# Kernel tuning notes

Measured on AMD Instinct MI355X. Metric: run time of the kernel, lower is better.

The kernel has to match this reference:

```python
import jax, jax.numpy as jnp
import numpy as np


def _kabsch_rmsd(p, c):
    # p, c: [N, 3]
    pm = jnp.mean(p, axis=0)  # [3]
    cm = jnp.mean(c, axis=0)  # [3]
    # 3x3 cross-covariance
    A = (p - pm).T @ (c - cm)
    U, S, Vt = jnp.linalg.svd(A, full_matrices=False)
    d = jnp.sign(jnp.linalg.det(A))
    # corr_mat = diag([1, 1, d]);  rotation = U @ corr_mat @ Vt
    scale = jnp.concatenate([jnp.ones((2,), dtype=p.dtype), d[None].astype(p.dtype)])
    R = U @ (scale[:, None] * Vt)  # [3,3]
    # translation = pm - R @ cm; aligned coords = (R @ c^T)^T + translation
    aligned = c @ R.T + (pm - R @ cm)
    sq = jnp.sum((p - aligned) ** 2, axis=1)  # [N]
    return jnp.sqrt(jnp.mean(sq))


def setup_inputs() -> dict:
    key = jax.random.key(0)
    k1, k2 = jax.random.split(key)
    B, N = 4096, 2048
    coords_pred = jax.random.normal(k1, (B, N, 3), dtype=jnp.float32)
    coords = jax.random.normal(k2, (B, N, 3), dtype=jnp.float32)
    return {"coords_pred": coords_pred, "coords": coords}


def reference(coords_pred, coords):
    # Batched Kabsch alignment + RMSD; default mode='global', return_all=False
    # -> mean over the per-sample RMSDs.
    rmsds = jax.vmap(_kabsch_rmsd)(coords_pred, coords)  # [B]
    return jnp.mean(rmsds)
```

## Files before the change

### kernel.cpp

```cpp
#include <hip/hip_runtime.h>
#include <math.h>

#define NPTS 2048
#define BLOCK 256
#define BPB 4
#define CHUNKS (NPTS / (64 * 4))

__global__ __launch_bounds__(BLOCK, 4) void kabsch_kernel(
    const float* __restrict__ P, const float* __restrict__ C,
    float* __restrict__ out, int B) {
  const int wave = threadIdx.x >> 6;
  const int lane = threadIdx.x & 63;
  const int b = blockIdx.x * BPB + wave;

  double rmsd = 0.0;
  if (b < B) {
    const float4* p4 = (const float4*)(P + (size_t)b * (NPTS * 3));
    const float4* c4 = (const float4*)(C + (size_t)b * (NPTS * 3));

    float acc[17];
#pragma unroll
    for (int i = 0; i < 17; i++) acc[i] = 0.f;

#define ACCUM(PA, PB, PQ, CA, CB, CQ)                                   \
  do {                                                                  \
    const float Px[4] = {PA.x, PA.w, PB.z, PQ.y};                       \
    const float Py[4] = {PA.y, PB.x, PB.w, PQ.z};                       \
    const float Pz[4] = {PA.z, PB.y, PQ.x, PQ.w};                       \
    const float Cx[4] = {CA.x, CA.w, CB.z, CQ.y};                       \
    const float Cy[4] = {CA.y, CB.x, CB.w, CQ.z};                       \
    const float Cz[4] = {CA.z, CB.y, CQ.x, CQ.w};                       \
    _Pragma("unroll")                                                   \
    for (int i = 0; i < 4; i++) {                                       \
      const float px = Px[i], py = Py[i], pz = Pz[i];                   \
      const float cx = Cx[i], cy = Cy[i], cz = Cz[i];                   \
      acc[0] += px; acc[1] += py; acc[2] += pz;                         \
      acc[3] += cx; acc[4] += cy; acc[5] += cz;                         \
      acc[6] += px * px + py * py + pz * pz;                            \
      acc[7] += cx * cx + cy * cy + cz * cz;                            \
      acc[8]  += px * cx; acc[9]  += px * cy; acc[10] += px * cz;       \
      acc[11] += py * cx; acc[12] += py * cy; acc[13] += py * cz;       \
      acc[14] += pz * cx; acc[15] += pz * cy; acc[16] += pz * cz;       \
    }                                                                   \
  } while (0)

    int base = 3 * lane;
    float4 pa = p4[base], pb = p4[base + 1], pq = p4[base + 2];
    float4 ca = c4[base], cb = c4[base + 1], cq = c4[base + 2];
#pragma unroll
    for (int k = 0; k < CHUNKS - 1; k++) {
      base += 64 * 3;
      const float4 npa = p4[base], npb = p4[base + 1], npq = p4[base + 2];
      const float4 nca = c4[base], ncb = c4[base + 1], ncq = c4[base + 2];
      __builtin_amdgcn_sched_barrier(0);
      ACCUM(pa, pb, pq, ca, cb, cq);
      pa = npa; pb = npb; pq = npq;
      ca = nca; cb = ncb; cq = ncq;
    }
    ACCUM(pa, pb, pq, ca, cb, cq);

#pragma unroll
    for (int off = 32; off > 0; off >>= 1) {
#pragma unroll
      for (int i = 0; i < 17; i++) acc[i] += __shfl_down(acc[i], off);
    }

    if (lane == 0) {
      double s[17];
#pragma unroll
      for (int i = 0; i < 17; i++) s[i] = (double)acc[i];
      const double invN = 1.0 / (double)NPTS;
      const double spx = s[0], spy = s[1], spz = s[2];
      const double scx = s[3], scy = s[4], scz = s[5];
      const double Ep = s[6] - (spx * spx + spy * spy + spz * spz) * invN;
      const double Ec = s[7] - (scx * scx + scy * scy + scz * scz) * invN;
      const double a00 = s[8]  - spx * scx * invN, a01 = s[9]  - spx * scy * invN, a02 = s[10] - spx * scz * invN;
      const double a10 = s[11] - spy * scx * invN, a11 = s[12] - spy * scy * invN, a12 = s[13] - spy * scz * invN;
      const double a20 = s[14] - spz * scx * invN, a21 = s[15] - spz * scy * invN, a22 = s[16] - spz * scz * invN;
      const double det = a00 * (a11 * a22 - a12 * a21)
                       - a01 * (a10 * a22 - a12 * a20)
                       + a02 * (a10 * a21 - a11 * a20);
      const double b00 = a00 * a00 + a10 * a10 + a20 * a20;
      const double b11 = a01 * a01 + a11 * a11 + a21 * a21;
      const double b22 = a02 * a02 + a12 * a12 + a22 * a22;
      const double b01 = a00 * a01 + a10 * a11 + a20 * a21;
      const double b02 = a00 * a02 + a10 * a12 + a20 * a22;
      const double b12 = a01 * a02 + a11 * a12 + a21 * a22;
      const double q = (b00 + b11 + b22) / 3.0;
      const double p1 = b01 * b01 + b02 * b02 + b12 * b12;
      const double d0 = b00 - q, d1 = b11 - q, d2 = b22 - q;
      const double p2 = d0 * d0 + d1 * d1 + d2 * d2 + 2.0 * p1;
      double e1, e2, e3;
      if (p2 < 1e-30) {
        e1 = e2 = e3 = q;
      } else {
        const double pp = sqrt(p2 / 6.0);
        const double inv = 1.0 / pp;
        const double c00 = d0 * inv, c11 = d1 * inv, c22 = d2 * inv;
        const double c01 = b01 * inv, c02 = b02 * inv, c12 = b12 * inv;
        double r = 0.5 * (c00 * (c11 * c22 - c12 * c12)
                        - c01 * (c01 * c22 - c12 * c02)
                        + c02 * (c01 * c12 - c11 * c02));
        r = fmin(1.0, fmax(-1.0, r));
        const double phi = acos(r) / 3.0;
        e1 = q + 2.0 * pp * cos(phi);
        e3 = q + 2.0 * pp * cos(phi + 2.0943951023931953);
        e2 = 3.0 * q - e1 - e3;
      }
      const double s1 = sqrt(fmax(e1, 0.0));
      const double s2 = sqrt(fmax(e2, 0.0));
      const double s3 = sqrt(fmax(e3, 0.0));
      const double dsign = (det > 0.0) ? 1.0 : ((det < 0.0) ? -1.0 : 0.0);
      const double trRS = s1 + s2 + dsign * s3;
      const double msd = (Ep + Ec - 2.0 * trRS) * invN;
      rmsd = sqrt(fmax(msd, 0.0));
    }
  }

  __shared__ double red[BPB];
  if (lane == 0) red[wave] = rmsd;
  __syncthreads();
  if (threadIdx.x == 0) {
    const double sum = red[0] + red[1] + red[2] + red[3];
    atomicAdd(out, (float)(sum / (double)B));
  }
}

extern "C" void kernel_launch(void* const* d_in, const int* in_sizes, int n_in,
                              void* d_out, int out_size, void* d_ws, size_t ws_size,
                              hipStream_t stream) {
  const float* P = (const float*)d_in[0];
  const float* C = (const float*)d_in[1];
  float* out = (float*)d_out;
  const int B = in_sizes[0] / (NPTS * 3);
  hipMemsetAsync(out, 0, sizeof(float), stream);
  kabsch_kernel<<<(B + BPB - 1) / BPB, BLOCK, 0, stream>>>(P, C, out, B);
}
```

Before: 217.2 us.

## Stage inputs through LDS with async global_load_lds double buffering

Replaces direct per-lane float4 global loads with global_load_lds transfers into per-wave double-buffered LDS, then reads each lane's 12 contiguous floats from LDS. Each wave now processes two batch samples sequentially, halving the grid, and launch bounds drop to 2 blocks per CU because of the 48KB LDS footprint. The intent is to keep more bytes in flight and get coalesced wide loads. The costs are an extra LDS round trip, manual waitcnt management, and lower occupancy on a kernel that is memory-bound.

```diff
diff --git a/kernel.cpp b/kernel.cpp
--- a/kernel.cpp
+++ b/kernel.cpp
@@ -3,24 +3,27 @@
 
 #define NPTS 2048
 #define BLOCK 256
-#define BPB 4
-#define CHUNKS (NPTS / (64 * 4))
+#define NW 4
+#define NB 2
+#define CHUNK_F 768
+#define NCHUNK (NPTS * 3 / CHUNK_F)
 
-__global__ __launch_bounds__(BLOCK, 4) void kabsch_kernel(
+#define GLD_LDS(gp, lp)                                                       \
+  __builtin_amdgcn_global_load_lds(                                           \
+      (const __attribute__((address_space(1))) void*)(gp),                    \
+      (__attribute__((address_space(3))) void*)(lp), 16, 0, 0)
+
+__global__ __launch_bounds__(BLOCK, 2) void kabsch_kernel(
     const float* __restrict__ P, const float* __restrict__ C,
     float* __restrict__ out, int B) {
   const int wave = threadIdx.x >> 6;
   const int lane = threadIdx.x & 63;
-  const int b = blockIdx.x * BPB + wave;
 
-  double rmsd = 0.0;
-  if (b < B) {
-    const float4* p4 = (const float4*)(P + (size_t)b * (NPTS * 3));
-    const float4* c4 = (const float4*)(C + (size_t)b * (NPTS * 3));
+  __shared__ float lds[NW][2][2 * CHUNK_F];
+  float* const buf0 = &lds[wave][0][0];
+  float* const buf1 = &lds[wave][1][0];
 
-    float acc[17];
-#pragma unroll
-    for (int i = 0; i < 17; i++) acc[i] = 0.f;
+  double rmsd_sum = 0.0;
 
 #define ACCUM(PA, PB, PQ, CA, CB, CQ)                                   \
   do {                                                                  \
@@ -44,81 +47,111 @@
     }                                                                   \
   } while (0)
 
-    int base = 3 * lane;
-    float4 pa = p4[base], pb = p4[base + 1], pq = p4[base + 2];
-    float4 ca = c4[base], cb = c4[base + 1], cq = c4[base + 2];
+#define STAGE(dst, kk)                                                  \
+  do {                                                                  \
+    const float* ps = pB + (kk) * CHUNK_F + lane * 4;                   \
+    const float* cs = cB + (kk) * CHUNK_F + lane * 4;                   \
+    GLD_LDS(ps,       (dst));                                           \
+    GLD_LDS(ps + 256, (dst) + 256);                                     \
+    GLD_LDS(ps + 512, (dst) + 512);                                     \
+    GLD_LDS(cs,       (dst) + 768);                                     \
+    GLD_LDS(cs + 256, (dst) + 1024);                                    \
+    GLD_LDS(cs + 512, (dst) + 1280);                                    \
+  } while (0)
+
+  for (int it = 0; it < NB; ++it) {
+    const int b = (blockIdx.x * NW + wave) * NB + it;
+    if (b < B) {
+      const float* pB = P + (size_t)b * (NPTS * 3);
+      const float* cB = C + (size_t)b * (NPTS * 3);
+
+      float acc[17];
 #pragma unroll
-    for (int k = 0; k < CHUNKS - 1; k++) {
-      base += 64 * 3;
-      const float4 npa = p4[base], npb = p4[base + 1], npq = p4[base + 2];
-      const float4 nca = c4[base], ncb = c4[base + 1], ncq = c4[base + 2];
-      __builtin_amdgcn_sched_barrier(0);
-      ACCUM(pa, pb, pq, ca, cb, cq);
-      pa = npa; pb = npb; pq = npq;
-      ca = nca; cb = ncb; cq = ncq;
-    }
-    ACCUM(pa, pb, pq, ca, cb, cq);
+      for (int i = 0; i < 17; i++) acc[i] = 0.f;
+
+      STAGE(buf0, 0);
+#pragma unroll
+      for (int k = 0; k < NCHUNK; ++k) {
+        float* const cur = (k & 1) ? buf1 : buf0;
+        float* const nxt = (k & 1) ? buf0 : buf1;
+        if (k + 1 < NCHUNK) {
+          asm volatile("s_waitcnt lgkmcnt(0)" ::: "memory");
+          STAGE(nxt, k + 1);
+          asm volatile("s_waitcnt vmcnt(6)" ::: "memory");
+        } else {
+          asm volatile("s_waitcnt vmcnt(0)" ::: "memory");
+        }
+        __builtin_amdgcn_sched_barrier(0);
+        const float4 pa = *(const float4*)(cur + 12 * lane);
+        const float4 pb = *(const float4*)(cur + 12 * lane + 4);
+        const float4 pq = *(const float4*)(cur + 12 * lane + 8);
+        const float4 ca = *(const float4*)(cur + 768 + 12 * lane);
+        const float4 cb = *(const float4*)(cur + 768 + 12 * lane + 4);
+        const float4 cq = *(const float4*)(cur + 768 + 12 * lane + 8);
+        ACCUM(pa, pb, pq, ca, cb, cq);
+      }
 
 #pragma unroll
-    for (int off = 32; off > 0; off >>= 1) {
+      for (int off = 32; off > 0; off >>= 1) {
 #pragma unroll
-      for (int i = 0; i < 17; i++) acc[i] += __shfl_down(acc[i], off);
-    }
+        for (int i = 0; i < 17; i++) acc[i] += __shfl_down(acc[i], off);
+      }
 
-    if (lane == 0) {
-      double s[17];
+      if (lane == 0) {
+        double s[17];
 #pragma unroll
-      for (int i = 0; i < 17; i++) s[i] = (double)acc[i];
-      const double invN = 1.0 / (double)NPTS;
-      const double spx = s[0], spy = s[1], spz = s[2];
-      const double scx = s[3], scy = s[4], scz = s[5];
-      const double Ep = s[6] - (spx * spx + spy * spy + spz * spz) * invN;
-      const double Ec = s[7] - (scx * scx + scy * scy + scz * scz) * invN;
-      const double a00 = s[8]  - spx * scx * invN, a01 = s[9]  - spx * scy * invN, a02 = s[10] - spx * scz * invN;
-      const double a10 = s[11] - spy * scx * invN, a11 = s[12] - spy * scy * invN, a12 = s[13] - spy * scz * invN;
-      const double a20 = s[14] - spz * scx * invN, a21 = s[15] - spz * scy * invN, a22 = s[16] - spz * scz * invN;
-      const double det = a00 * (a11 * a22 - a12 * a21)
-                       - a01 * (a10 * a22 - a12 * a20)
-                       + a02 * (a10 * a21 - a11 * a20);
-      const double b00 = a00 * a00 + a10 * a10 + a20 * a20;
-      const double b11 = a01 * a01 + a11 * a11 + a21 * a21;
-      const double b22 = a02 * a02 + a12 * a12 + a22 * a22;
-      const double b01 = a00 * a01 + a10 * a11 + a20 * a21;
-      const double b02 = a00 * a02 + a10 * a12 + a20 * a22;
-      const double b12 = a01 * a02 + a11 * a12 + a21 * a22;
-      const double q = (b00 + b11 + b22) / 3.0;
-      const double p1 = b01 * b01 + b02 * b02 + b12 * b12;
-      const double d0 = b00 - q, d1 = b11 - q, d2 = b22 - q;
-      const double p2 = d0 * d0 + d1 * d1 + d2 * d2 + 2.0 * p1;
-      double e1, e2, e3;
-      if (p2 < 1e-30) {
-        e1 = e2 = e3 = q;
-      } else {
-        const double pp = sqrt(p2 / 6.0);
-        const double inv = 1.0 / pp;
-        const double c00 = d0 * inv, c11 = d1 * inv, c22 = d2 * inv;
-        const double c01 = b01 * inv, c02 = b02 * inv, c12 = b12 * inv;
-        double r = 0.5 * (c00 * (c11 * c22 - c12 * c12)
-                        - c01 * (c01 * c22 - c12 * c02)
-                        + c02 * (c01 * c12 - c11 * c02));
-        r = fmin(1.0, fmax(-1.0, r));
-        const double phi = acos(r) / 3.0;
-        e1 = q + 2.0 * pp * cos(phi);
-        e3 = q + 2.0 * pp * cos(phi + 2.0943951023931953);
-        e2 = 3.0 * q - e1 - e3;
+        for (int i = 0; i < 17; i++) s[i] = (double)acc[i];
+        const double invN = 1.0 / (double)NPTS;
+        const double spx = s[0], spy = s[1], spz = s[2];
+        const double scx = s[3], scy = s[4], scz = s[5];
+        const double Ep = s[6] - (spx * spx + spy * spy + spz * spz) * invN;
+        const double Ec = s[7] - (scx * scx + scy * scy + scz * scz) * invN;
+        const double a00 = s[8]  - spx * scx * invN, a01 = s[9]  - spx * scy * invN, a02 = s[10] - spx * scz * invN;
+        const double a10 = s[11] - spy * scx * invN, a11 = s[12] - spy * scy * invN, a12 = s[13] - spy * scz * invN;
+        const double a20 = s[14] - spz * scx * invN, a21 = s[15] - spz * scy * invN, a22 = s[16] - spz * scz * invN;
+        const double det = a00 * (a11 * a22 - a12 * a21)
+                         - a01 * (a10 * a22 - a12 * a20)
+                         + a02 * (a10 * a21 - a11 * a20);
+        const double b00 = a00 * a00 + a10 * a10 + a20 * a20;
+        const double b11 = a01 * a01 + a11 * a11 + a21 * a21;
+        const double b22 = a02 * a02 + a12 * a12 + a22 * a22;
+        const double b01 = a00 * a01 + a10 * a11 + a20 * a21;
+        const double b02 = a00 * a02 + a10 * a12 + a20 * a22;
+        const double b12 = a01 * a02 + a11 * a12 + a21 * a22;
+        const double q = (b00 + b11 + b22) / 3.0;
+        const double p1 = b01 * b01 + b02 * b02 + b12 * b12;
+        const double d0 = b00 - q, d1 = b11 - q, d2 = b22 - q;
+        const double p2 = d0 * d0 + d1 * d1 + d2 * d2 + 2.0 * p1;
+        double e1, e2, e3;
+        if (p2 < 1e-30) {
+          e1 = e2 = e3 = q;
+        } else {
+          const double pp = sqrt(p2 / 6.0);
+          const double inv = 1.0 / pp;
+          const double c00 = d0 * inv, c11 = d1 * inv, c22 = d2 * inv;
+          const double c01 = b01 * inv, c02 = b02 * inv, c12 = b12 * inv;
+          double r = 0.5 * (c00 * (c11 * c22 - c12 * c12)
+                          - c01 * (c01 * c22 - c12 * c02)
+                          + c02 * (c01 * c12 - c11 * c02));
+          r = fmin(1.0, fmax(-1.0, r));
+          const double phi = acos(r) / 3.0;
+          e1 = q + 2.0 * pp * cos(phi);
+          e3 = q + 2.0 * pp * cos(phi + 2.0943951023931953);
+          e2 = 3.0 * q - e1 - e3;
+        }
+        const double s1 = sqrt(fmax(e1, 0.0));
+        const double s2 = sqrt(fmax(e2, 0.0));
+        const double s3 = sqrt(fmax(e3, 0.0));
+        const double dsign = (det > 0.0) ? 1.0 : ((det < 0.0) ? -1.0 : 0.0);
+        const double trRS = s1 + s2 + dsign * s3;
+        const double msd = (Ep + Ec - 2.0 * trRS) * invN;
+        rmsd_sum += sqrt(fmax(msd, 0.0));
       }
-      const double s1 = sqrt(fmax(e1, 0.0));
-      const double s2 = sqrt(fmax(e2, 0.0));
-      const double s3 = sqrt(fmax(e3, 0.0));
-      const double dsign = (det > 0.0) ? 1.0 : ((det < 0.0) ? -1.0 : 0.0);
-      const double trRS = s1 + s2 + dsign * s3;
-      const double msd = (Ep + Ec - 2.0 * trRS) * invN;
-      rmsd = sqrt(fmax(msd, 0.0));
     }
   }
 
-  __shared__ double red[BPB];
-  if (lane == 0) red[wave] = rmsd;
+  __shared__ double red[NW];
+  if (lane == 0) red[wave] = rmsd_sum;
   __syncthreads();
   if (threadIdx.x == 0) {
     const double sum = red[0] + red[1] + red[2] + red[3];
@@ -134,5 +167,5 @@
   float* out = (float*)d_out;
   const int B = in_sizes[0] / (NPTS * 3);
   hipMemsetAsync(out, 0, sizeof(float), stream);
-  kabsch_kernel<<<(B + BPB - 1) / BPB, BLOCK, 0, stream>>>(P, C, out, B);
+  kabsch_kernel<<<(B + NW * NB - 1) / (NW * NB), BLOCK, 0, stream>>>(P, C, out, B);
 }
```

New measurement: 218.4 us. No clear change (+0.6%).

## Split each batch item across four waves with shared-memory partial reduction

Applied to the files above, without the earlier changes.

Each batch item was handled by a single 64-lane wave. It is now split across four waves, each covering a quarter of the points, so a 1024-thread block handles four items. Partial sums for the 17 statistics go through shared memory, and four threads finish the eigen solve and combine their results with shuffles before one atomic per block. The explicit software prefetch with sched_barrier is dropped in favour of two straight load/accumulate iterations, relying on the extra waves in flight to hide memory latency. The cost is an extra block-wide barrier and a shared-memory reduction step.

```diff
diff --git a/kernel.cpp b/kernel.cpp
--- a/kernel.cpp
+++ b/kernel.cpp
@@ -2,25 +2,21 @@
 #include <math.h>
 
 #define NPTS 2048
-#define BLOCK 256
+#define BLOCK 1024
 #define BPB 4
-#define CHUNKS (NPTS / (64 * 4))
+#define WPB 4
 
-__global__ __launch_bounds__(BLOCK, 4) void kabsch_kernel(
+__global__ __launch_bounds__(BLOCK, 8) void kabsch_kernel(
     const float* __restrict__ P, const float* __restrict__ C,
     float* __restrict__ out, int B) {
-  const int wave = threadIdx.x >> 6;
+  const int w = threadIdx.x >> 6;
   const int lane = threadIdx.x & 63;
-  const int b = blockIdx.x * BPB + wave;
+  const int batch = blockIdx.x * BPB + (w >> 2);
+  const int slice = w & 3;
 
-  double rmsd = 0.0;
-  if (b < B) {
-    const float4* p4 = (const float4*)(P + (size_t)b * (NPTS * 3));
-    const float4* c4 = (const float4*)(C + (size_t)b * (NPTS * 3));
-
-    float acc[17];
+  float acc[17];
 #pragma unroll
-    for (int i = 0; i < 17; i++) acc[i] = 0.f;
+  for (int i = 0; i < 17; i++) acc[i] = 0.f;
 
 #define ACCUM(PA, PB, PQ, CA, CB, CQ)                                   \
   do {                                                                  \
@@ -44,31 +40,43 @@
     }                                                                   \
   } while (0)
 
-    int base = 3 * lane;
-    float4 pa = p4[base], pb = p4[base + 1], pq = p4[base + 2];
-    float4 ca = c4[base], cb = c4[base + 1], cq = c4[base + 2];
+  if (batch < B) {
+    const float4* p4 = (const float4*)P + (size_t)batch * 1536 + slice * 384 + 3 * lane;
+    const float4* c4 = (const float4*)C + (size_t)batch * 1536 + slice * 384 + 3 * lane;
 #pragma unroll
-    for (int k = 0; k < CHUNKS - 1; k++) {
-      base += 64 * 3;
-      const float4 npa = p4[base], npb = p4[base + 1], npq = p4[base + 2];
-      const float4 nca = c4[base], ncb = c4[base + 1], ncq = c4[base + 2];
-      __builtin_amdgcn_sched_barrier(0);
+    for (int it = 0; it < 2; ++it) {
+      const float4 pa = p4[it * 192],     pb = p4[it * 192 + 1], pq = p4[it * 192 + 2];
+      const float4 ca = c4[it * 192],     cb = c4[it * 192 + 1], cq = c4[it * 192 + 2];
       ACCUM(pa, pb, pq, ca, cb, cq);
-      pa = npa; pb = npb; pq = npq;
-      ca = nca; cb = ncb; cq = ncq;
     }
-    ACCUM(pa, pb, pq, ca, cb, cq);
+  }
 
 #pragma unroll
-    for (int off = 32; off > 0; off >>= 1) {
+  for (int off = 32; off > 0; off >>= 1) {
 #pragma unroll
-      for (int i = 0; i < 17; i++) acc[i] += __shfl_down(acc[i], off);
-    }
+    for (int i = 0; i < 17; i++) acc[i] += __shfl_down(acc[i], off);
+  }
 
-    if (lane == 0) {
+  __shared__ float red[BPB * WPB][17];
+  if (lane == 0) {
+#pragma unroll
+    for (int i = 0; i < 17; i++) red[w][i] = acc[i];
+  }
+  __syncthreads();
+
+  double v = 0.0;
+  if (threadIdx.x < BPB) {
+    const int t = threadIdx.x;
+    const int bt = blockIdx.x * BPB + t;
+    if (bt < B) {
       double s[17];
 #pragma unroll
-      for (int i = 0; i < 17; i++) s[i] = (double)acc[i];
+      for (int i = 0; i < 17; i++) {
+        float f = red[t * WPB][i];
+#pragma unroll
+        for (int j = 1; j < WPB; j++) f += red[t * WPB + j][i];
+        s[i] = (double)f;
+      }
       const double invN = 1.0 / (double)NPTS;
       const double spx = s[0], spy = s[1], spz = s[2];
       const double scx = s[3], scy = s[4], scz = s[5];
@@ -113,17 +121,12 @@
       const double dsign = (det > 0.0) ? 1.0 : ((det < 0.0) ? -1.0 : 0.0);
       const double trRS = s1 + s2 + dsign * s3;
       const double msd = (Ep + Ec - 2.0 * trRS) * invN;
-      rmsd = sqrt(fmax(msd, 0.0));
+      v = sqrt(fmax(msd, 0.0));
     }
   }
-
-  __shared__ double red[BPB];
-  if (lane == 0) red[wave] = rmsd;
-  __syncthreads();
-  if (threadIdx.x == 0) {
-    const double sum = red[0] + red[1] + red[2] + red[3];
-    atomicAdd(out, (float)(sum / (double)B));
-  }
+  v += __shfl_down(v, 2);
+  v += __shfl_down(v, 1);
+  if (threadIdx.x == 0) atomicAdd(out, (float)(v / (double)B));
 }
 
 extern "C" void kernel_launch(void* const* d_in, const int* in_sizes, int n_in,
```

Result: no change. 221.4 us (+1.9%).
